# Kernel optimization log

Hardware: AMD Instinct MI355X
Metric: run time of the kernel (lower is better)

Reference implementation:

```python
import jax, jax.numpy as jnp
import numpy as np

IN_CH = 512
OUT_CH = 3
W_DIM = 512
CLAMP = 256.0

# setup_filter([1,3,3,1]): outer product, normalized to sum 1 (separable FIR)
_f1 = np.array([1.0, 3.0, 3.0, 1.0], dtype=np.float32)
_f2 = np.outer(_f1, _f1)
_f2 = _f2 / _f2.sum()
FIR = jnp.asarray(_f2)  # [4,4], symmetric so flipping is a no-op


def setup_inputs() -> dict:
    key = jax.random.key(0)
    ks = jax.random.split(key, 5)
    return {
        "x": jax.random.normal(ks[0], (8, IN_CH, 128, 128), jnp.float32),
        "w": jax.random.normal(ks[1], (8, W_DIM), jnp.float32),
        "skip": jax.random.normal(ks[2], (8, OUT_CH, 64, 64), jnp.float32),
        "affine_w": jax.random.normal(ks[3], (IN_CH, W_DIM), jnp.float32),
        "affine_b": jnp.ones((IN_CH,), jnp.float32),  # bias_init=1
        "weight": jax.random.normal(ks[4], (OUT_CH, IN_CH, 1, 1), jnp.float32),
        "bias": jnp.zeros((OUT_CH,), jnp.float32),
    }


def _upsample2d(s):
    # upfirdn2d.upsample2d(up=2): zero-insert, pad, FIR filter, gain = up**2 = 4.
    # lax lhs_dilation=2 gives 2H-1 samples (no trailing zero); torch ref pads
    # (2,1) on the 2H-length sequence -> equivalent lax padding is (2,2).
    C = s.shape[1]
    k = jnp.tile((FIR * 4.0)[None, None], (C, 1, 1, 1))  # [C,1,4,4] depthwise
    return jax.lax.conv_general_dilated(
        s, k, window_strides=(1, 1), padding=((2, 2), (2, 2)),
        lhs_dilation=(2, 2),
        dimension_numbers=("NCHW", "OIHW", "NCHW"),
        feature_group_count=C,
    )


def reference(x, w, skip, affine_w, affine_b, weight, bias):
    # affine DenseLayer: default activation='lrelu' (alpha=0.2, gain=sqrt(2))
    affine_gain = 1.0 / np.sqrt(W_DIM)
    styles = jax.nn.leaky_relu(w @ (affine_w * affine_gain).T + affine_b, 0.2)
    styles = styles * np.float32(np.sqrt(2.0))  # [B, IN_CH]

    # modulated 1x1 conv, demodulate=False, groups=batch ->
    # out[b,o,h,w] = sum_i (weight[o,i]*wg) * styles[b,i] * x[b,i,h,w]
    wm = weight[:, :, 0, 0] * (1.0 / IN_CH)  # weight_gain = 1/in_channels
    y = jnp.einsum("oi,bi,bihw->bohw", wm, styles, x)

    # bias_act: linear act + clamp
    y = jnp.clip(y + bias[None, :, None, None], -CLAMP, CLAMP)

    return y + _upsample2d(skip)
```

## Files before the change

kernel.cpp:

```cpp
#include <hip/hip_runtime.h>
#include <math.h>


#define IN_CH 512
#define OUT_CH 3
#define NPIX 16384
#define NB 8

__global__ __launch_bounds__(256) void coeff_kernel(
    const float* __restrict__ w, const float* __restrict__ aw,
    const float* __restrict__ ab, const float* __restrict__ wt,
    float* __restrict__ coeff) {
  const int b  = blockIdx.x >> 6;
  const int rg = blockIdx.x & 63;
  const int tid = threadIdx.x;
  __shared__ float wv[512];
  wv[tid]       = w[b * 512 + tid];
  wv[tid + 256] = w[b * 512 + 256 + tid];
  __syncthreads();
  const int wave = tid >> 6, lane = tid & 63;
  const float gain = 1.0f / sqrtf(512.0f);
  #pragma unroll
  for (int r = 0; r < 2; ++r) {
    const int i = rg * 8 + wave * 2 + r;
    const float* row = aw + (size_t)i * 512;
    float s = 0.f;
    #pragma unroll
    for (int k = 0; k < 8; ++k) s += row[lane + 64 * k] * wv[lane + 64 * k];
    #pragma unroll
    for (int off = 32; off >= 1; off >>= 1) s += __shfl_xor(s, off, 64);
    if (lane == 0) {
      float v = s * gain + ab[i];
      v = (v > 0.f ? v : 0.2f * v) * 1.41421356237f;
      #pragma unroll
      for (int o = 0; o < OUT_CH; ++o)
        coeff[b * (OUT_CH * IN_CH) + o * IN_CH + i] =
            wt[o * IN_CH + i] * (1.0f / 512.0f) * v;
    }
  }
}

__global__ __launch_bounds__(256) void main_kernel(
    const float* __restrict__ x, const float* __restrict__ coeff,
    const float* __restrict__ bias, const float* __restrict__ skip,
    float* __restrict__ out) {
  const int b   = blockIdx.x >> 7;
  const int g   = blockIdx.x & 127;
  const int p0  = g * 128;
  const int tid = threadIdx.x;
  const int col   = tid & 31;
  const int split = tid >> 5;

  __shared__ float lds_c[8 * 64 * 4];
  for (int idx = tid; idx < 2048; idx += 256) {
    const int s = idx >> 8, rem = idx & 255, k = rem >> 2, o = rem & 3;
    lds_c[idx] = (o < 3)
        ? coeff[b * (OUT_CH * IN_CH) + o * IN_CH + s * 64 + k]
        : 0.f;
  }

  float up[3] = {0.f, 0.f, 0.f};
  if (tid < 128) {
    const int p = p0 + tid;
    const int yy = p >> 7, xx = p & 127;
    int iy0, ix0; float wy0, wy1, wx0, wx1;
    if (yy & 1) { iy0 = (yy - 1) >> 1; wy0 = 3.f; wy1 = 1.f; }
    else        { iy0 = (yy >> 1) - 1; wy0 = 1.f; wy1 = 3.f; }
    if (xx & 1) { ix0 = (xx - 1) >> 1; wx0 = 3.f; wx1 = 1.f; }
    else        { ix0 = (xx >> 1) - 1; wx0 = 1.f; wx1 = 3.f; }
    const float wyx00 = wy0 * wx0 * (1.f / 16.f), wyx01 = wy0 * wx1 * (1.f / 16.f);
    const float wyx10 = wy1 * wx0 * (1.f / 16.f), wyx11 = wy1 * wx1 * (1.f / 16.f);
    const bool y0ok = (iy0 >= 0), y1ok = (iy0 + 1 < 64);
    const bool x0ok = (ix0 >= 0), x1ok = (ix0 + 1 < 64);
    #pragma unroll
    for (int o = 0; o < OUT_CH; ++o) {
      const float* sp = skip + ((size_t)(b * OUT_CH + o)) * 4096;
      float s00 = (y0ok && x0ok) ? sp[iy0 * 64 + ix0]           : 0.f;
      float s01 = (y0ok && x1ok) ? sp[iy0 * 64 + ix0 + 1]       : 0.f;
      float s10 = (y1ok && x0ok) ? sp[(iy0 + 1) * 64 + ix0]     : 0.f;
      float s11 = (y1ok && x1ok) ? sp[(iy0 + 1) * 64 + ix0 + 1] : 0.f;
      up[o] = wyx00 * s00 + wyx01 * s01 + wyx10 * s10 + wyx11 * s11;
    }
  }

  __syncthreads();

  const float* xp = x + ((size_t)(b * IN_CH + split * 64)) * NPIX + p0 + col * 4;
  const float* cp = lds_c + split * 256;

  float acc[12];
  #pragma unroll
  for (int j = 0; j < 12; ++j) acc[j] = 0.f;

  #pragma unroll 8
  for (int k = 0; k < 64; ++k) {
    float4 xv = *reinterpret_cast<const float4*>(xp + (size_t)k * NPIX);
    float4 c4 = *reinterpret_cast<const float4*>(cp + k * 4);
    acc[0] += c4.x * xv.x; acc[1]  += c4.x * xv.y; acc[2]  += c4.x * xv.z; acc[3]  += c4.x * xv.w;
    acc[4] += c4.y * xv.x; acc[5]  += c4.y * xv.y; acc[6]  += c4.y * xv.z; acc[7]  += c4.y * xv.w;
    acc[8] += c4.z * xv.x; acc[9]  += c4.z * xv.y; acc[10] += c4.z * xv.z; acc[11] += c4.z * xv.w;
  }

  #pragma unroll
  for (int j = 0; j < 12; ++j) acc[j] += __shfl_xor(acc[j], 32, 64);

  __shared__ float red[4][32][13];
  const int wave = tid >> 6, lane = tid & 63;
  if (lane < 32) {
    #pragma unroll
    for (int j = 0; j < 12; ++j) red[wave][lane][j] = acc[j];
  }
  __syncthreads();

  if (tid < 128) {
    const int c = tid >> 2, s = tid & 3;
    #pragma unroll
    for (int o = 0; o < OUT_CH; ++o) {
      const int j = o * 4 + s;
      float v = red[0][c][j] + red[1][c][j] + red[2][c][j] + red[3][c][j] + bias[o];
      v = fminf(fmaxf(v, -256.f), 256.f);
      out[((size_t)(b * OUT_CH + o)) * NPIX + p0 + tid] = v + up[o];
    }
  }
}

extern "C" void kernel_launch(void* const* d_in, const int* in_sizes, int n_in,
                              void* d_out, int out_size, void* d_ws, size_t ws_size,
                              hipStream_t stream) {
  const float* x        = (const float*)d_in[0];
  const float* w        = (const float*)d_in[1];
  const float* skip     = (const float*)d_in[2];
  const float* affine_w = (const float*)d_in[3];
  const float* affine_b = (const float*)d_in[4];
  const float* weight   = (const float*)d_in[5];
  const float* bias     = (const float*)d_in[6];
  float* out   = (float*)d_out;
  float* coeff = (float*)d_ws;

  coeff_kernel<<<512, 256, 0, stream>>>(w, affine_w, affine_b, weight, coeff);
  main_kernel<<<NB * 128, 256, 0, stream>>>(x, coeff, bias, skip, out);
}
```

Baseline: 52.11 us.

## Fuse coeff and main kernels with a grid-wide atomic barrier

Merges the style/coefficient kernel into the main kernel. Each of the 1024 blocks computes four style rows, publishes them, and signals an atomic counter. Blocks then spin until every block has arrived before loading coefficients and running the channel reduction, with the skip upsample placed before the wait to hide it. This saves a kernel launch and the inter-kernel gap, but it adds a memset launch and relies on all 1024 blocks being co-resident (launch_bounds 256,8), otherwise it deadlocks. Unroll is also reduced from 8 to 4.

```diff
diff --git a/kernel.cpp b/kernel.cpp
--- a/kernel.cpp
+++ b/kernel.cpp
@@ -7,22 +7,28 @@
 #define NPIX 16384
 #define NB 8
 
-__global__ __launch_bounds__(256) void coeff_kernel(
-    const float* __restrict__ w, const float* __restrict__ aw,
+__global__ __launch_bounds__(256, 8) void fused_kernel(
+    const float* __restrict__ x, const float* __restrict__ w,
+    const float* __restrict__ skip, const float* __restrict__ aw,
     const float* __restrict__ ab, const float* __restrict__ wt,
-    float* __restrict__ coeff) {
-  const int b  = blockIdx.x >> 6;
-  const int rg = blockIdx.x & 63;
+    const float* __restrict__ bias, float* __restrict__ out,
+    int* __restrict__ ctr, float* __restrict__ coeff) {
+  const int bid = blockIdx.x;
   const int tid = threadIdx.x;
+  const int b   = bid >> 7;
+  const int g   = bid & 127;
+  const int p0  = g * 128;
+
   __shared__ float wv[512];
+  __shared__ float lds_c[8 * 64 * 4];
+  __shared__ float red[4][32][13];
+
   wv[tid]       = w[b * 512 + tid];
   wv[tid + 256] = w[b * 512 + 256 + tid];
   __syncthreads();
   const int wave = tid >> 6, lane = tid & 63;
-  const float gain = 1.0f / sqrtf(512.0f);
-  #pragma unroll
-  for (int r = 0; r < 2; ++r) {
-    const int i = rg * 8 + wave * 2 + r;
+  {
+    const int i = g * 4 + wave;
     const float* row = aw + (size_t)i * 512;
     float s = 0.f;
     #pragma unroll
@@ -30,7 +36,7 @@
     #pragma unroll
     for (int off = 32; off >= 1; off >>= 1) s += __shfl_xor(s, off, 64);
     if (lane == 0) {
-      float v = s * gain + ab[i];
+      float v = s * (1.0f / sqrtf(512.0f)) + ab[i];
       v = (v > 0.f ? v : 0.2f * v) * 1.41421356237f;
       #pragma unroll
       for (int o = 0; o < OUT_CH; ++o)
@@ -38,26 +44,10 @@
             wt[o * IN_CH + i] * (1.0f / 512.0f) * v;
     }
   }
-}
-
-__global__ __launch_bounds__(256) void main_kernel(
-    const float* __restrict__ x, const float* __restrict__ coeff,
-    const float* __restrict__ bias, const float* __restrict__ skip,
-    float* __restrict__ out) {
-  const int b   = blockIdx.x >> 7;
-  const int g   = blockIdx.x & 127;
-  const int p0  = g * 128;
-  const int tid = threadIdx.x;
-  const int col   = tid & 31;
-  const int split = tid >> 5;
-
-  __shared__ float lds_c[8 * 64 * 4];
-  for (int idx = tid; idx < 2048; idx += 256) {
-    const int s = idx >> 8, rem = idx & 255, k = rem >> 2, o = rem & 3;
-    lds_c[idx] = (o < 3)
-        ? coeff[b * (OUT_CH * IN_CH) + o * IN_CH + s * 64 + k]
-        : 0.f;
-  }
+  __threadfence();
+  __syncthreads();
+  if (tid == 0)
+    __hip_atomic_fetch_add(ctr, 1, __ATOMIC_RELEASE, __HIP_MEMORY_SCOPE_AGENT);
 
   float up[3] = {0.f, 0.f, 0.f};
   if (tid < 128) {
@@ -83,6 +73,23 @@
     }
   }
 
+  if (tid == 0) {
+    while (__hip_atomic_load(ctr, __ATOMIC_ACQUIRE, __HIP_MEMORY_SCOPE_AGENT) < 1024) {
+      __builtin_amdgcn_s_sleep(16);
+    }
+  }
+  __syncthreads();
+  __threadfence();
+
+  const int col   = tid & 31;
+  const int split = tid >> 5;
+
+  for (int idx = tid; idx < 2048; idx += 256) {
+    const int s = idx >> 8, rem = idx & 255, k = rem >> 2, o = rem & 3;
+    lds_c[idx] = (o < 3)
+        ? coeff[b * (OUT_CH * IN_CH) + o * IN_CH + s * 64 + k]
+        : 0.f;
+  }
   __syncthreads();
 
   const float* xp = x + ((size_t)(b * IN_CH + split * 64)) * NPIX + p0 + col * 4;
@@ -92,7 +99,7 @@
   #pragma unroll
   for (int j = 0; j < 12; ++j) acc[j] = 0.f;
 
-  #pragma unroll 8
+  #pragma unroll 4
   for (int k = 0; k < 64; ++k) {
     float4 xv = *reinterpret_cast<const float4*>(xp + (size_t)k * NPIX);
     float4 c4 = *reinterpret_cast<const float4*>(cp + k * 4);
@@ -104,8 +111,6 @@
   #pragma unroll
   for (int j = 0; j < 12; ++j) acc[j] += __shfl_xor(acc[j], 32, 64);
 
-  __shared__ float red[4][32][13];
-  const int wave = tid >> 6, lane = tid & 63;
   if (lane < 32) {
     #pragma unroll
     for (int j = 0; j < 12; ++j) red[wave][lane][j] = acc[j];
@@ -135,8 +140,11 @@
   const float* weight   = (const float*)d_in[5];
   const float* bias     = (const float*)d_in[6];
   float* out   = (float*)d_out;
-  float* coeff = (float*)d_ws;
 
-  coeff_kernel<<<512, 256, 0, stream>>>(w, affine_w, affine_b, weight, coeff);
-  main_kernel<<<NB * 128, 256, 0, stream>>>(x, coeff, bias, skip, out);
+  int*   ctr   = (int*)d_ws;
+  float* coeff = (float*)((char*)d_ws + 256);
+
+  hipMemsetAsync(ctr, 0, sizeof(int), stream);
+  fused_kernel<<<NB * 128, 256, 0, stream>>>(
+      x, w, skip, affine_w, affine_b, weight, bias, out, ctr, coeff);
 }
```

Result: slower. 207.2 us (+297.6%).
